# Performance work log

Hardware: AMD Instinct MI355X
Metric: run time of the kernel (lower is better)

The kernel has to match this reference:

```python
import jax, jax.numpy as jnp
import numpy as np

T1, T2, T3 = 0.05, 0.1, 0.15
EPS = 1e-8  # matches torch cosine_similarity clamp


def _propagate(x, t):
    # GEmbedding: cosine-similarity adjacency  [B,N,F] -> [B,N,N]
    xn = x / jnp.maximum(jnp.linalg.norm(x, axis=-1, keepdims=True), EPS)
    adj = jnp.einsum('bnf,bmf->bnm', xn, xn)
    # F.threshold(adj, t, 0): keep values strictly greater than t
    adj = jnp.where(adj > t, adj, 0.0)
    # GraphAdjNorm: D^{-1/2} A D^{-1/2} via row/col broadcast (same math as
    # the original diag-matmul, without materializing diagonal matrices)
    d = jnp.sum(adj, axis=-1)              # [B,N]
    inv_sqrt = 1.0 / jnp.sqrt(d)           # [B,N]
    adj = adj * inv_sqrt[..., :, None] * inv_sqrt[..., None, :]
    return jnp.einsum('bnm,bmf->bnf', adj, x)


def setup_inputs() -> dict:
    key = jax.random.key(0)
    k1, k2 = jax.random.split(key)
    B, N, F = 8, 2048, 128
    x = jax.random.normal(k1, (B, N, F), dtype=jnp.float32)
    weight = jax.random.normal(k2, (F, F), dtype=jnp.float32) * 0.05
    return {"x": x, "weight": weight}


def reference(x, weight):
    res = x
    h = x
    for t in (T1, T2, T3):
        h = _propagate(h, t)
    h = jax.lax.stop_gradient(h)  # torch.no_grad() block
    return jnp.einsum('bnf,fo->bno', h + res, weight)
```

## Files before the change

kernel.cpp:

```cpp
#include <hip/hip_runtime.h>
#include <hip/hip_bf16.h>
#include <cstdint>

#define BQ 8
#define NQ 2048
#define FQ 128
#define NG (NQ * 16)
#define HSS 256.0f

typedef __attribute__((ext_vector_type(8))) short short8;
typedef __attribute__((ext_vector_type(4))) float f32x4;
typedef __attribute__((ext_vector_type(8))) unsigned short us8;
typedef __attribute__((ext_vector_type(2))) unsigned int u32x2;

__device__ __forceinline__ unsigned short f2bf(float f) {
    union { float f; unsigned int u; } c; c.f = f;
    unsigned int u = c.u;
    u = (u + 0x7FFFu + ((u >> 16) & 1u)) >> 16;
    return (unsigned short)u;
}
__device__ __forceinline__ float bf2f(unsigned short u) {
    union { unsigned int i; float f; } c; c.i = (unsigned int)u << 16; return c.f;
}
__device__ __forceinline__ unsigned int pk8lo(float a, float b, unsigned int old) {
    return (unsigned int)__builtin_amdgcn_cvt_pk_fp8_f32(a, b, (int)old, false);
}
__device__ __forceinline__ unsigned int pk8hi(float a, float b, unsigned int old) {
    return (unsigned int)__builtin_amdgcn_cvt_pk_fp8_f32(a, b, (int)old, true);
}


__global__ __launch_bounds__(256) void k_rownorm(const float* __restrict__ h,
                                                 unsigned short* __restrict__ xnF) {
    int t = threadIdx.x;
    int rl = t >> 4, j = t & 15;
    size_t row = (size_t)blockIdx.x * 16 + rl;
    const float* hr = h + row * FQ + j * 8;
    float v[8];
    #pragma unroll
    for (int e = 0; e < 8; ++e) v[e] = hr[e];
    float s = 0.f;
    #pragma unroll
    for (int e = 0; e < 8; ++e) s += v[e] * v[e];
    s += __shfl_xor(s, 1, 64);
    s += __shfl_xor(s, 2, 64);
    s += __shfl_xor(s, 4, 64);
    s += __shfl_xor(s, 8, 64);
    float inv = 1.0f / fmaxf(sqrtf(s), 1e-8f);
    us8 u;
    #pragma unroll
    for (int e = 0; e < 8; ++e) u[e] = f2bf(v[e] * inv);
    *(us8*)(xnF + (size_t)blockIdx.x * 2048 + j * 128 + rl * 8) = u;
}

__global__ __launch_bounds__(512) void k_adj(const unsigned short* __restrict__ xnF,
                                             unsigned char* __restrict__ adjF,
                                             float* __restrict__ dpart, float t) {
    __shared__ unsigned short As[16384];
    __shared__ unsigned short Bsh[16384];

    int bid = blockIdx.x;
    int blk = (bid & 7) * (int)(gridDim.x >> 3) + (bid >> 3);
    int bb  = blk >> 8;
    int ij  = blk & 255;
    int I   = ij >> 4, J = ij & 15;
    int tid = threadIdx.x;
    int wid = tid >> 6, lane = tid & 63;
    int wr = wid >> 1, wc = wid & 1;
    int g = lane >> 4, c = lane & 15;

    const unsigned short* xb = xnF + (size_t)bb * NQ * FQ;
    int rowb = I * 128 + wr * 32;
    int colb = J * 128 + wc * 64;

    {
        const unsigned short* srcA = xb + (size_t)(I * 8) * 2048;
        const unsigned short* srcB = xb + (size_t)(J * 8) * 2048;
        #pragma unroll
        for (int it = 0; it < 4; ++it) {
            __builtin_amdgcn_global_load_lds(
                (const __attribute__((address_space(1))) void*)(srcA + (size_t)(it * 512 + tid) * 8),
                (__attribute__((address_space(3))) void*)(As + (it * 512 + wid * 64) * 8),
                16, 0, 0);
            __builtin_amdgcn_global_load_lds(
                (const __attribute__((address_space(1))) void*)(srcB + (size_t)(it * 512 + tid) * 8),
                (__attribute__((address_space(3))) void*)(Bsh + (it * 512 + wid * 64) * 8),
                16, 0, 0);
        }
    }
    __syncthreads();

    short8 a[2][4];
    #pragma unroll
    for (int mi = 0; mi < 2; ++mi)
        #pragma unroll
        for (int ks = 0; ks < 4; ++ks)
            a[mi][ks] = *(const short8*)(As + (wr * 2 + mi) * 2048 + (ks * 4 + g) * 128 + c * 8);

    f32x4 acc[2][4];
    #pragma unroll
    for (int mi = 0; mi < 2; ++mi)
        #pragma unroll
        for (int ni = 0; ni < 4; ++ni) acc[mi][ni] = (f32x4){0.f, 0.f, 0.f, 0.f};

    #pragma unroll
    for (int ni = 0; ni < 4; ++ni) {
        short8 b[4];
        #pragma unroll
        for (int ks = 0; ks < 4; ++ks)
            b[ks] = *(const short8*)(Bsh + (wc * 4 + ni) * 2048 + (ks * 4 + g) * 128 + c * 8);
        #pragma unroll
        for (int mi = 0; mi < 2; ++mi)
            #pragma unroll
            for (int ks = 0; ks < 4; ++ks)
                acc[mi][ni] = __builtin_amdgcn_mfma_f32_16x16x32_bf16(a[mi][ks], b[ks], acc[mi][ni], 0, 0, 0);
    }

    unsigned char* adjb = adjF + (size_t)bb * NQ * NQ;
    __shared__ float dsm[2][128];
    float dl[2][4];
    #pragma unroll
    for (int mi = 0; mi < 2; ++mi)
        #pragma unroll
        for (int r = 0; r < 4; ++r) dl[mi][r] = 0.f;

    #pragma unroll
    for (int mi = 0; mi < 2; ++mi)
        #pragma unroll
        for (int ni = 0; ni < 4; ++ni) {
            f32x4 v = acc[mi][ni];
            float x0 = (v[0] > t) ? v[0] : 0.0f;
            float x1 = (v[1] > t) ? v[1] : 0.0f;
            float x2 = (v[2] > t) ? v[2] : 0.0f;
            float x3 = (v[3] > t) ? v[3] : 0.0f;
            dl[mi][0] += x0; dl[mi][1] += x1; dl[mi][2] += x2; dl[mi][3] += x3;
            unsigned int u = pk8lo(x0, x1, 0u);
            u = pk8hi(x2, x3, u);
            *(unsigned int*)(adjb + (size_t)((colb >> 4) + ni) * NG
                                  + (size_t)((rowb >> 3) + mi * 2 + (g >> 1)) * 128
                                  + c * 8 + (g & 1) * 4) = u;
        }

    #pragma unroll
    for (int mi = 0; mi < 2; ++mi)
        #pragma unroll
        for (int r = 0; r < 4; ++r) {
            float s = dl[mi][r];
            s += __shfl_xor(s, 1, 64);
            s += __shfl_xor(s, 2, 64);
            s += __shfl_xor(s, 4, 64);
            s += __shfl_xor(s, 8, 64);
            dl[mi][r] = s;
        }
    if (c == 0) {
        #pragma unroll
        for (int mi = 0; mi < 2; ++mi)
            #pragma unroll
            for (int r = 0; r < 4; ++r)
                dsm[wc][wr * 32 + mi * 16 + g * 4 + r] = dl[mi][r];
    }
    __syncthreads();
    if (tid < 128)
        dpart[((size_t)J * 8 + bb) * NQ + I * 128 + tid] = dsm[0][tid] + dsm[1][tid];
}

__global__ __launch_bounds__(256) void k_prep_f32(const float* __restrict__ h,
                                                  const float* __restrict__ dpart,
                                                  float* __restrict__ isq,
                                                  unsigned char* __restrict__ hsF) {
    __shared__ float tile[32][129];
    __shared__ float iv[32];
    int r0 = blockIdx.x * 32;
    int bb = r0 >> 11;
    int m0 = r0 & (NQ - 1);
    int tid = threadIdx.x;
    if (tid < 32) {
        float s = 0.f;
        #pragma unroll
        for (int j = 0; j < 16; ++j)
            s += dpart[((size_t)j * 8 + bb) * NQ + m0 + tid];
        float v = 1.0f / sqrtf(s);
        iv[tid] = v;
        isq[r0 + tid] = v;
    }
    #pragma unroll
    for (int it = 0; it < 16; ++it) {
        int idx = tid + it * 256;
        int mi = idx >> 7, f = idx & 127;
        tile[mi][f] = h[(size_t)(r0 + mi) * FQ + f];
    }
    __syncthreads();
    unsigned char* hb = hsF + (size_t)bb * NQ * FQ;
    #pragma unroll
    for (int it = 0; it < 2; ++it) {
        int p = tid + it * 256;
        int f = p & 127, mc = p >> 7;
        float sv[8];
        #pragma unroll
        for (int e = 0; e < 8; ++e)
            sv[e] = tile[mc * 8 + e][f] * iv[mc * 8 + e] * HSS;
        u32x2 u;
        u[0] = pk8hi(sv[2], sv[3], pk8lo(sv[0], sv[1], 0u));
        u[1] = pk8hi(sv[6], sv[7], pk8lo(sv[4], sv[5], 0u));
        *(u32x2*)(hb + (size_t)((m0 >> 3) + mc) * 1024 + f * 8) = u;
    }
}

__global__ __launch_bounds__(256) void k_prep_bf16(const unsigned short* __restrict__ h,
                                                   const float* __restrict__ dpart,
                                                   float* __restrict__ isq,
                                                   unsigned char* __restrict__ hsF) {
    __shared__ float tile[32][129];
    __shared__ float iv[32];
    int r0 = blockIdx.x * 32;
    int bb = r0 >> 11;
    int m0 = r0 & (NQ - 1);
    int tid = threadIdx.x;
    if (tid < 32) {
        float s = 0.f;
        #pragma unroll
        for (int j = 0; j < 16; ++j)
            s += dpart[((size_t)j * 8 + bb) * NQ + m0 + tid];
        float v = 1.0f / sqrtf(s);
        iv[tid] = v;
        isq[r0 + tid] = v;
    }
    #pragma unroll
    for (int it = 0; it < 16; ++it) {
        int idx = tid + it * 256;
        int mi = idx >> 7, f = idx & 127;
        tile[mi][f] = bf2f(h[(size_t)(r0 + mi) * FQ + f]);
    }
    __syncthreads();
    unsigned char* hb = hsF + (size_t)bb * NQ * FQ;
    #pragma unroll
    for (int it = 0; it < 2; ++it) {
        int p = tid + it * 256;
        int f = p & 127, mc = p >> 7;
        float sv[8];
        #pragma unroll
        for (int e = 0; e < 8; ++e)
            sv[e] = tile[mc * 8 + e][f] * iv[mc * 8 + e] * HSS;
        u32x2 u;
        u[0] = pk8hi(sv[2], sv[3], pk8lo(sv[0], sv[1], 0u));
        u[1] = pk8hi(sv[6], sv[7], pk8lo(sv[4], sv[5], 0u));
        *(u32x2*)(hb + (size_t)((m0 >> 3) + mc) * 1024 + f * 8) = u;
    }
}

template<bool LAST>
__global__ __launch_bounds__(512) void k_gemm3(const unsigned char* __restrict__ adjF,
                                               const unsigned char* __restrict__ hsF,
                                               const float* __restrict__ isq,
                                               unsigned short* __restrict__ hout,
                                               unsigned short* __restrict__ xnF) {
    __shared__ unsigned char Bs[32768];
    __shared__ float red[64][128];

    int bid = blockIdx.x;
    int lb = (bid & 7) * 32 + (bid >> 3);
    int bb = lb >> 5;
    int rt = lb & 31;
    int row0g = rt * 64;
    int tid = threadIdx.x;
    int wid = tid >> 6, lane = tid & 63;
    int g = lane >> 4, c = lane & 15;
    int rg = wid >> 2, kh = wid & 3;
    int wrow = row0g + rg * 32;

    const unsigned char* adjr = adjF + (size_t)bb * NQ * NQ + (size_t)(wrow >> 4) * NG;
    const unsigned char* hb   = hsF + (size_t)bb * NQ * FQ;

    f32x4 acc[2][8];
    #pragma unroll
    for (int mi = 0; mi < 2; ++mi)
        #pragma unroll
        for (int i = 0; i < 8; ++i) acc[mi][i] = (f32x4){0.f, 0.f, 0.f, 0.f};

    int khr = wid >> 1;
    int wlo = wid & 1;

    for (int ph = 0; ph < 8; ++ph) {
        __syncthreads();
        {
            const unsigned char* src = hb + (size_t)(khr * 64 + ph * 8) * 1024 + wlo * 1024;
            unsigned char* dst = Bs + khr * 8192 + wlo * 1024;
            #pragma unroll
            for (int it = 0; it < 4; ++it) {
                __builtin_amdgcn_global_load_lds(
                    (const __attribute__((address_space(1))) void*)(src + it * 2048 + lane * 16),
                    (__attribute__((address_space(3))) void*)(dst + it * 2048),
                    16, 0, 0);
            }
        }
        __syncthreads();
        #pragma unroll
        for (int kk2 = 0; kk2 < 2; ++kk2) {
            int mstep = kh * 16 + ph * 2 + kk2;
            long a0 = *(const long*)(adjr + (size_t)(mstep * 4 + g) * 128 + c * 8);
            long a1 = *(const long*)(adjr + NG + (size_t)(mstep * 4 + g) * 128 + c * 8);
            #pragma unroll
            for (int ct = 0; ct < 8; ++ct) {
                long bfr = *(const long*)(Bs + kh * 8192 + kk2 * 4096 + g * 1024 + (ct * 16 + c) * 8);
                acc[0][ct] = __builtin_amdgcn_mfma_f32_16x16x32_fp8_fp8(a0, bfr, acc[0][ct], 0, 0, 0);
                acc[1][ct] = __builtin_amdgcn_mfma_f32_16x16x32_fp8_fp8(a1, bfr, acc[1][ct], 0, 0, 0);
            }
        }
    }

    __syncthreads();
    #pragma unroll
    for (int s = 0; s < 4; ++s) {
        if (kh == s) {
            #pragma unroll
            for (int mi = 0; mi < 2; ++mi)
                #pragma unroll
                for (int ct = 0; ct < 8; ++ct)
                    #pragma unroll
                    for (int r = 0; r < 4; ++r) {
                        int rl = rg * 32 + mi * 16 + g * 4 + r;
                        if (s == 0) red[rl][ct * 16 + c] = acc[mi][ct][r];
                        else        red[rl][ct * 16 + c] += acc[mi][ct][r];
                    }
        }
        __syncthreads();
    }

    int rl = tid >> 3;
    int j  = tid & 7;
    int n  = row0g + rl;
    float scale = isq[(size_t)bb * NQ + n] * (1.0f / HSS);
    float v[16];
    float s = 0.f;
    #pragma unroll
    for (int e = 0; e < 16; ++e) {
        float x = red[rl][j * 16 + e] * scale;
        v[e] = x;
        s += x * x;
    }
    s += __shfl_xor(s, 1, 64);
    s += __shfl_xor(s, 2, 64);
    s += __shfl_xor(s, 4, 64);
    float inv = 1.0f / fmaxf(sqrtf(s), 1e-8f);

    us8 h0, h1;
    #pragma unroll
    for (int e = 0; e < 8; ++e) { h0[e] = f2bf(v[e]); h1[e] = f2bf(v[8 + e]); }
    unsigned short* hrow = hout + ((size_t)bb * NQ + n) * FQ + j * 16;
    *(us8*)hrow = h0;
    *(us8*)(hrow + 8) = h1;

    if constexpr (!LAST) {
        us8 u0, u1;
        #pragma unroll
        for (int e = 0; e < 8; ++e) { u0[e] = f2bf(v[e] * inv); u1[e] = f2bf(v[8 + e] * inv); }
        unsigned short* xd = xnF + (size_t)bb * NQ * FQ + (size_t)(n >> 4) * 2048
                                 + (j * 2) * 128 + (n & 15) * 8;
        *(us8*)xd = u0;
        *(us8*)(xd + 128) = u1;
    }
}

__global__ __launch_bounds__(256) void k_out(const unsigned short* __restrict__ h3,
                                             const float* __restrict__ x,
                                             const float* __restrict__ W,
                                             float* __restrict__ out) {
    __shared__ float hx[8][128];
    int r0 = blockIdx.x * 8;
    int tid = threadIdx.x;
    #pragma unroll
    for (int it = 0; it < 4; ++it) {
        int idx = tid + it * 256;
        int ri = idx >> 7, f = idx & 127;
        size_t gi = (size_t)(r0 + ri) * FQ + f;
        hx[ri][f] = bf2f(h3[gi]) + x[gi];
    }
    __syncthreads();
    int o = tid & 127, half = tid >> 7;
    float acc[4] = {0.f, 0.f, 0.f, 0.f};
    for (int f = 0; f < 128; ++f) {
        float wv = W[f * 128 + o];
        #pragma unroll
        for (int j = 0; j < 4; ++j)
            acc[j] += hx[half * 4 + j][f] * wv;
    }
    #pragma unroll
    for (int j = 0; j < 4; ++j)
        out[(size_t)(r0 + half * 4 + j) * FQ + o] = acc[j];
}

extern "C" void kernel_launch(void* const* d_in, const int* in_sizes, int n_in,
                              void* d_out, int out_size, void* d_ws, size_t ws_size,
                              hipStream_t stream) {
    const float* x = (const float*)d_in[0];
    const float* W = (const float*)d_in[1];
    float* out = (float*)d_out;
    char* ws = (char*)d_ws;

    const size_t CS   = (size_t)BQ * NQ * FQ;
    const size_t oADJ = 0;
    const size_t oXN  = oADJ + (size_t)BQ * NQ * NQ;
    const size_t oHST = oXN  + CS * 2;
    const size_t oD   = oHST + CS;
    const size_t oISQ = oD   + (size_t)16 * BQ * NQ * 4;
    const size_t oHA  = oISQ + (size_t)BQ * NQ * 4;
    const size_t oHB  = oHA  + CS * 2;
    const size_t need = oHB  + CS * 2;
    if (ws_size < need) return;

    unsigned char*  adjF = (unsigned char*)(ws + oADJ);
    unsigned short* xnF  = (unsigned short*)(ws + oXN);
    unsigned char*  hsF  = (unsigned char*)(ws + oHST);
    float* dpart = (float*)(ws + oD);
    float* isq   = (float*)(ws + oISQ);
    unsigned short* hA = (unsigned short*)(ws + oHA);
    unsigned short* hB = (unsigned short*)(ws + oHB);

    const float ts[3] = {0.05f, 0.1f, 0.15f};

    k_rownorm<<<BQ * NQ / 16, 256, 0, stream>>>(x, xnF);
    k_adj<<<BQ * 256, 512, 0, stream>>>(xnF, adjF, dpart, ts[0]);
    k_prep_f32<<<BQ * NQ / 32, 256, 0, stream>>>(x, dpart, isq, hsF);
    k_gemm3<false><<<BQ * 32, 512, 0, stream>>>(adjF, hsF, isq, hA, xnF);
    k_adj<<<BQ * 256, 512, 0, stream>>>(xnF, adjF, dpart, ts[1]);
    k_prep_bf16<<<BQ * NQ / 32, 256, 0, stream>>>(hA, dpart, isq, hsF);
    k_gemm3<false><<<BQ * 32, 512, 0, stream>>>(adjF, hsF, isq, hB, xnF);
    k_adj<<<BQ * 256, 512, 0, stream>>>(xnF, adjF, dpart, ts[2]);
    k_prep_bf16<<<BQ * NQ / 32, 256, 0, stream>>>(hB, dpart, isq, hsF);
    k_gemm3<true><<<BQ * 32, 512, 0, stream>>>(adjF, hsF, isq, hA, xnF);

    k_out<<<BQ * NQ / 8, 256, 0, stream>>>(hA, x, W, out);
}
```

Measured before the change: 146.2 us.

## Exploit adjacency symmetry: compute upper-triangle tiles and write transposed mirror

The adjacency kernel now launches only the upper-triangular 128x128 tile pairs (136 per batch instead of 256), since the cosine-similarity matrix is symmetric. For off-diagonal tiles it transposes the fp8 result through shared memory, which is unioned with the B operand buffer, and writes the mirror tile. It also computes column sums to fill the mirrored degree partials. This roughly halves the MFMA work and input loads in k_adj, at the cost of extra LDS traffic, an additional barrier, byte-shuffle work, and a serial loop to decode the tile index.

Measured after the change: 141.6 us. -3.2%, faster.

```diff
diff --git a/kernel.cpp b/kernel.cpp
--- a/kernel.cpp
+++ b/kernel.cpp
@@ -12,6 +12,7 @@
 typedef __attribute__((ext_vector_type(4))) float f32x4;
 typedef __attribute__((ext_vector_type(8))) unsigned short us8;
 typedef __attribute__((ext_vector_type(2))) unsigned int u32x2;
+typedef __attribute__((ext_vector_type(4))) unsigned int u32x4;
 
 __device__ __forceinline__ unsigned short f2bf(float f) {
     union { float f; unsigned int u; } c; c.f = f;
@@ -57,13 +58,18 @@
                                              unsigned char* __restrict__ adjF,
                                              float* __restrict__ dpart, float t) {
     __shared__ unsigned short As[16384];
-    __shared__ unsigned short Bsh[16384];
+    __shared__ union { unsigned short Bsh[16384];
+                       unsigned char  T2[128 * 132]; } ub;
+    __shared__ float dsm[2][128];
+    __shared__ float csm[2][128];
 
     int bid = blockIdx.x;
-    int blk = (bid & 7) * (int)(gridDim.x >> 3) + (bid >> 3);
-    int bb  = blk >> 8;
-    int ij  = blk & 255;
-    int I   = ij >> 4, J = ij & 15;
+    int bb = bid & 7;
+    int pr = bid >> 3;
+    int I = 0;
+    { int p = pr; while (p >= 16 - I) { p -= 16 - I; ++I; } pr = p; }
+    int J = I + pr;
+
     int tid = threadIdx.x;
     int wid = tid >> 6, lane = tid & 63;
     int wr = wid >> 1, wc = wid & 1;
@@ -84,7 +90,7 @@
                 16, 0, 0);
             __builtin_amdgcn_global_load_lds(
                 (const __attribute__((address_space(1))) void*)(srcB + (size_t)(it * 512 + tid) * 8),
-                (__attribute__((address_space(3))) void*)(Bsh + (it * 512 + wid * 64) * 8),
+                (__attribute__((address_space(3))) void*)(ub.Bsh + (it * 512 + wid * 64) * 8),
                 16, 0, 0);
         }
     }
@@ -108,7 +114,7 @@
         short8 b[4];
         #pragma unroll
         for (int ks = 0; ks < 4; ++ks)
-            b[ks] = *(const short8*)(Bsh + (wc * 4 + ni) * 2048 + (ks * 4 + g) * 128 + c * 8);
+            b[ks] = *(const short8*)(ub.Bsh + (wc * 4 + ni) * 2048 + (ks * 4 + g) * 128 + c * 8);
         #pragma unroll
         for (int mi = 0; mi < 2; ++mi)
             #pragma unroll
@@ -116,9 +122,11 @@
                 acc[mi][ni] = __builtin_amdgcn_mfma_f32_16x16x32_bf16(a[mi][ks], b[ks], acc[mi][ni], 0, 0, 0);
     }
 
+    __syncthreads();
+
     unsigned char* adjb = adjF + (size_t)bb * NQ * NQ;
-    __shared__ float dsm[2][128];
     float dl[2][4];
+    float csl[4] = {0.f, 0.f, 0.f, 0.f};
     #pragma unroll
     for (int mi = 0; mi < 2; ++mi)
         #pragma unroll
@@ -134,11 +142,17 @@
             float x2 = (v[2] > t) ? v[2] : 0.0f;
             float x3 = (v[3] > t) ? v[3] : 0.0f;
             dl[mi][0] += x0; dl[mi][1] += x1; dl[mi][2] += x2; dl[mi][3] += x3;
+            csl[ni] += x0 + x1 + x2 + x3;
             unsigned int u = pk8lo(x0, x1, 0u);
             u = pk8hi(x2, x3, u);
             *(unsigned int*)(adjb + (size_t)((colb >> 4) + ni) * NG
                                   + (size_t)((rowb >> 3) + mi * 2 + (g >> 1)) * 128
                                   + c * 8 + (g & 1) * 4) = u;
+            if (I != J) {
+                int colL = wc * 64 + ni * 16 + c;
+                int rowL = wr * 32 + mi * 16 + g * 4;
+                *(unsigned int*)(ub.T2 + colL * 132 + rowL) = u;
+            }
         }
 
     #pragma unroll
@@ -159,9 +173,53 @@
             for (int r = 0; r < 4; ++r)
                 dsm[wc][wr * 32 + mi * 16 + g * 4 + r] = dl[mi][r];
     }
-    __syncthreads();
+    if (I != J) {
+        #pragma unroll
+        for (int ni = 0; ni < 4; ++ni) {
+            float s = csl[ni];
+            s += __shfl_xor(s, 16, 64);
+            s += __shfl_xor(s, 32, 64);
+            csl[ni] = s;
+        }
+        if (lane < 16) {
+            #pragma unroll
+            for (int ni = 0; ni < 4; ++ni)
+                csm[wr & 1][wc * 64 + ni * 16 + lane] = csl[ni];
+        }
+    }
+    __syncthreads();
+    if (I != J && (wr >= 2) && lane < 16) {
+        #pragma unroll
+        for (int ni = 0; ni < 4; ++ni)
+            csm[wr & 1][wc * 64 + ni * 16 + lane] += csl[ni];
+    }
+    __syncthreads();
+
     if (tid < 128)
         dpart[((size_t)J * 8 + bb) * NQ + I * 128 + tid] = dsm[0][tid] + dsm[1][tid];
+    if (I != J) {
+        if (tid < 128)
+            dpart[((size_t)I * 8 + bb) * NQ + J * 128 + tid] = csm[0][tid] + csm[1][tid];
+        int ng = wid;
+        int mg = lane >> 2;
+        int part = lane & 3;
+        unsigned int w[8];
+        #pragma unroll
+        for (int ml = 0; ml < 8; ++ml)
+            w[ml] = *(const unsigned int*)(ub.T2 + (mg * 8 + ml) * 132 + ng * 16 + part * 4);
+        unsigned int o32[8];
+        #pragma unroll
+        for (int i = 0; i < 4; ++i)
+            #pragma unroll
+            for (int h = 0; h < 2; ++h)
+                o32[i * 2 + h] = ((w[h * 4 + 0] >> (8 * i)) & 0xFFu)
+                               | (((w[h * 4 + 1] >> (8 * i)) & 0xFFu) << 8)
+                               | (((w[h * 4 + 2] >> (8 * i)) & 0xFFu) << 16)
+                               | (((w[h * 4 + 3] >> (8 * i)) & 0xFFu) << 24);
+        unsigned char* dst = adjb + (size_t)(I * 8 + ng) * NG + (size_t)(J * 16 + mg) * 128 + part * 32;
+        *(u32x4*)dst        = (u32x4){o32[0], o32[1], o32[2], o32[3]};
+        *(u32x4*)(dst + 16) = (u32x4){o32[4], o32[5], o32[6], o32[7]};
+    }
 }
 
 __global__ __launch_bounds__(256) void k_prep_f32(const float* __restrict__ h,
@@ -419,13 +477,13 @@
     const float ts[3] = {0.05f, 0.1f, 0.15f};
 
     k_rownorm<<<BQ * NQ / 16, 256, 0, stream>>>(x, xnF);
-    k_adj<<<BQ * 256, 512, 0, stream>>>(xnF, adjF, dpart, ts[0]);
+    k_adj<<<BQ * 136, 512, 0, stream>>>(xnF, adjF, dpart, ts[0]);
     k_prep_f32<<<BQ * NQ / 32, 256, 0, stream>>>(x, dpart, isq, hsF);
     k_gemm3<false><<<BQ * 32, 512, 0, stream>>>(adjF, hsF, isq, hA, xnF);
-    k_adj<<<BQ * 256, 512, 0, stream>>>(xnF, adjF, dpart, ts[1]);
+    k_adj<<<BQ * 136, 512, 0, stream>>>(xnF, adjF, dpart, ts[1]);
     k_prep_bf16<<<BQ * NQ / 32, 256, 0, stream>>>(hA, dpart, isq, hsF);
     k_gemm3<false><<<BQ * 32, 512, 0, stream>>>(adjF, hsF, isq, hB, xnF);
-    k_adj<<<BQ * 256, 512, 0, stream>>>(xnF, adjF, dpart, ts[2]);
+    k_adj<<<BQ * 136, 512, 0, stream>>>(xnF, adjF, dpart, ts[2]);
     k_prep_bf16<<<BQ * NQ / 32, 256, 0, stream>>>(hB, dpart, isq, hsF);
     k_gemm3<true><<<BQ * 32, 512, 0, stream>>>(adjF, hsF, isq, hA, xnF);
 
```
